# Kernel tuning notes

Measured on AMD Instinct MI355X. Metric: run time of the kernel, lower is better.

The kernel has to match this reference:

```python
import jax, jax.numpy as jnp
import numpy as np

CH = 512
NUM_GROUPS = 32
EPS = 1e-6

def _xavier(key, shape):
    fan_in, fan_out = shape[1], shape[0]
    limit = np.sqrt(6.0 / (fan_in + fan_out))
    return jax.random.uniform(key, shape, jnp.float32, -limit, limit)

def setup_inputs() -> dict:
    key = jax.random.key(0)
    ks = jax.random.split(key, 6)
    B, C, H, W = 32, CH, 32, 32
    x = jax.random.normal(ks[0], (B, C, H, W), jnp.float32)
    # 1x1 conv weights stored as [C_out, C_in]; biases zero (per initialize())
    wq = _xavier(ks[1], (C, C)); wk = _xavier(ks[2], (C, C))
    wv = _xavier(ks[3], (C, C)); wp = _xavier(ks[4], (C, C))
    bq = jnp.zeros((C,)); bk = jnp.zeros((C,)); bv = jnp.zeros((C,)); bp = jnp.zeros((C,))
    gn_w = jnp.ones((C,)); gn_b = jnp.zeros((C,))
    return {"x": x, "gn_w": gn_w, "gn_b": gn_b,
            "wq": wq, "bq": bq, "wk": wk, "bk": bk,
            "wv": wv, "bv": bv, "wp": wp, "bp": bp}

def _group_norm(x, w, b):
    B, C, H, W = x.shape
    g = NUM_GROUPS
    xg = x.reshape(B, g, C // g, H, W)
    mean = xg.mean(axis=(2, 3, 4), keepdims=True)
    var = xg.var(axis=(2, 3, 4), keepdims=True)
    xn = ((xg - mean) * jax.lax.rsqrt(var + EPS)).reshape(B, C, H, W)
    return xn * w[None, :, None, None] + b[None, :, None, None]

def reference(x, gn_w, gn_b, wq, bq, wk, bk, wv, bv, wp, bp):
    B, C, H, W = x.shape
    h = _group_norm(x, gn_w, gn_b)
    hf = h.reshape(B, C, H * W)  # [B, C, N]
    # 1x1 convs == per-pixel linear over channels
    q = jnp.einsum('oc,bcn->bno', wq, hf) + bq  # [B, N, C]
    k = jnp.einsum('oc,bcn->bon', wk, hf) + bk[None, :, None]  # [B, C, N]
    v = jnp.einsum('oc,bcn->bno', wv, hf) + bv  # [B, N, C]
    attn = jnp.einsum('bqc,bck->bqk', q, k) * (C ** -0.5)  # [B, N, N]
    attn = jax.nn.softmax(attn, axis=-1)
    out = jnp.einsum('bqk,bkc->bqc', attn, v)  # [B, N, C]
    out = jnp.einsum('oc,bnc->bon', wp, out) + bp[None, :, None]  # [B, C, N]
    return x + out.reshape(B, C, H, W)
```

## Files before the change

### kernel.cpp

```cpp
#include <hip/hip_runtime.h>


#define C_DIM 512
#define N_PIX 1024
#define BATCH 32
#define CPG 16
#define EPS 1e-6f
#define SCALE 0.044194173824159216f
#define ESTRIDE 66
#define ESTRU   72

typedef unsigned short u16;
typedef __attribute__((ext_vector_type(8))) short bf16x8;
typedef __attribute__((ext_vector_type(4))) float f32x4;
typedef __attribute__((ext_vector_type(2))) float f32x2;

static __device__ __forceinline__ float bf2f(u16 u) {
    union { unsigned int i; float f; } v; v.i = ((unsigned int)u) << 16; return v.f;
}
static __device__ __forceinline__ u16 f2bf(float f) {
    union { float f; unsigned int i; } v; v.f = f;
    unsigned int r = v.i + 0x7fffu + ((v.i >> 16) & 1u);
    return (u16)(r >> 16);
}

static __device__ __forceinline__ void gl_lds16(const u16* g, u16* l) {
    __builtin_amdgcn_global_load_lds(
        (const __attribute__((address_space(1))) unsigned int*)g,
        (__attribute__((address_space(3))) unsigned int*)l,
        16, 0, 0);
}

#define BAR()   __builtin_amdgcn_s_barrier()
#define SCHED() __builtin_amdgcn_sched_barrier(0x7)

__global__ __launch_bounds__(256) void prep_kernel(
        const float* __restrict__ wq, const float* __restrict__ wk,
        const float* __restrict__ wv, const float* __restrict__ wp,
        u16* __restrict__ out, const float* __restrict__ x,
        float* __restrict__ stats) {
    int blk = blockIdx.x;
    if (blk < 1024) {
        int i = blk * 256 + threadIdx.x;
        int mat = i >> 16;
        const float* src = (mat == 0) ? wq : (mat == 1) ? wk : (mat == 2) ? wv : wp;
        float4 v = ((const float4*)src)[i & 65535];
        ushort4 o;
        o.x = f2bf(v.x); o.y = f2bf(v.y); o.z = f2bf(v.z); o.w = f2bf(v.w);
        *(ushort4*)&out[(size_t)i * 4] = o;
        return;
    }
    blk -= 1024;
    int b = blk >> 5, g = blk & 31;
    const float4* xv = (const float4*)(x + ((size_t)(b * C_DIM + g * CPG)) * N_PIX);
    int tid = threadIdx.x;
    float s = 0.f, sq = 0.f;
#pragma unroll 4
    for (int i = tid; i < (CPG * N_PIX) / 4; i += 256) {
        float4 v = xv[i];
        s  += v.x + v.y + v.z + v.w;
        sq += v.x * v.x + v.y * v.y + v.z * v.z + v.w * v.w;
    }
#pragma unroll
    for (int m = 1; m < 64; m <<= 1) {
        s += __shfl_xor(s, m);
        sq += __shfl_xor(sq, m);
    }
    __shared__ float rs[4], rq[4];
    int wv_ = tid >> 6;
    if ((tid & 63) == 0) { rs[wv_] = s; rq[wv_] = sq; }
    __syncthreads();
    if (tid == 0) {
        float S = rs[0] + rs[1] + rs[2] + rs[3];
        float Q = rq[0] + rq[1] + rq[2] + rq[3];
        float mean = S * (1.0f / (CPG * N_PIX));
        float var  = Q * (1.0f / (CPG * N_PIX)) - mean * mean;
        stats[blk * 2] = mean;
        stats[blk * 2 + 1] = rsqrtf(var + EPS);
    }
}

__global__ __launch_bounds__(256) void gnt_kernel(
        const float* __restrict__ x, const float* __restrict__ gw,
        const float* __restrict__ gb, const float* __restrict__ stats,
        u16* __restrict__ h) {
    int blk = blockIdx.x;
    int b = blk >> 4, nc = blk & 15;
    int n0 = nc * 64;
    __shared__ u16 T[64 * 520];
    int tid = threadIdx.x;
    int cq = tid >> 4;
    int n4 = tid & 15;
    const float* xb = x + (size_t)b * C_DIM * N_PIX + n0;
#pragma unroll 4
    for (int pass = 0; pass < 32; ++pass) {
        int c = pass * 16 + cq;
        int g = c >> 4;
        float mean = stats[(b * 32 + g) * 2];
        float inv  = stats[(b * 32 + g) * 2 + 1];
        float sc = gw[c] * inv;
        float sh = gb[c] - mean * sc;
        float4 v = *(const float4*)(xb + (size_t)c * N_PIX + n4 * 4);
        int nn = n4 * 4;
        T[(nn + 0) * 520 + c] = f2bf(v.x * sc + sh);
        T[(nn + 1) * 520 + c] = f2bf(v.y * sc + sh);
        T[(nn + 2) * 520 + c] = f2bf(v.z * sc + sh);
        T[(nn + 3) * 520 + c] = f2bf(v.w * sc + sh);
    }
    __syncthreads();
    u16* hb = h + ((size_t)b * N_PIX + n0) * C_DIM;
    int rr = tid >> 5;
    int cc = (tid & 31) * 16;
#pragma unroll
    for (int p = 0; p < 8; ++p) {
        int n = p * 8 + rr;
        bf16x8 v0 = *(const bf16x8*)&T[n * 520 + cc];
        bf16x8 v1 = *(const bf16x8*)&T[n * 520 + cc + 8];
        *(bf16x8*)&hb[(size_t)n * C_DIM + cc] = v0;
        *(bf16x8*)&hb[(size_t)n * C_DIM + cc + 8] = v1;
    }
}


#define MM(mq, nq) do { \
    _Pragma("unroll") \
    for (int t_ = 0; t_ < 4; ++t_) { \
        _Pragma("unroll") \
        for (int n_ = 0; n_ < 2; ++n_) { \
            _Pragma("unroll") \
            for (int ks_ = 0; ks_ < 2; ++ks_) \
                acc[(mq)*4 + t_][(nq)*2 + n_] = \
                    __builtin_amdgcn_mfma_f32_16x16x32_bf16( \
                        af[t_][ks_], bf[(nq)*2 + n_][ks_], \
                        acc[(mq)*4 + t_][(nq)*2 + n_], 0, 0, 0); \
        } \
    } \
} while (0)

template <int MODE, int NT>
__global__ __launch_bounds__(512, 2) void gemm_kernel(
        const u16* __restrict__ A, const u16* __restrict__ A2,
        const u16* __restrict__ B, const u16* __restrict__ B2,
        void* __restrict__ Cv, void* __restrict__ Cv2,
        const float* __restrict__ bias, const float* __restrict__ bias2,
        const float* __restrict__ xres, int K,
        int rsA, int rsB, int rsC,
        long long bsA, long long bsB, long long bsC,
        int nx, int ny) {
    const int nwg = 256 * NT;

    const u16* tgA[2]; const u16* tgB[2];
    void* tout[2]; const float* tbi[2];
    int tcb[2], tcolb[2], trowb[2];
#pragma unroll
    for (int tt = 0; tt < NT; ++tt) {
        int flat = blockIdx.x + tt * 256;
        int t = (flat & 7) * (nwg >> 3) + (flat >> 3);
        int bx = t % nx, by = (t / nx) % ny, bz = t / (nx * ny);
        int b = bz;
        const u16 *gA, *gB;
        void* out = Cv;
        const float* bi = bias;
        if (MODE == 0) {
            int mat = bz & 1; b = bz >> 1;
            gA = A + (size_t)b * bsA + (size_t)by * 256 * rsA;
            gB = B + (size_t)mat * 262144 + (size_t)bx * 256 * rsB;
            out = mat ? Cv2 : Cv;
            bi = mat ? bias2 : bias;
        } else if (MODE == 2) {
            gA = A + (size_t)b * bsA + (size_t)by * 256 * rsA;
            gB = B + (size_t)b * bsB + (size_t)bx * 256 * rsB;
            out = (b >= 16) ? Cv2 : Cv;
        } else if (MODE == 3) {
            gA = ((b >= 16) ? A2 : A) + (size_t)(b & 15) * bsA + (size_t)by * 256 * rsA;
            gB = B + (size_t)b * bsB + (size_t)bx * 256 * rsB;
            out = (b >= 16) ? Cv2 : Cv;
        } else if (MODE == 4) {
            gA = A + (size_t)by * 256 * rsA;
            gB = ((b >= 16) ? B2 : B) + (size_t)(b & 15) * bsB + (size_t)bx * 256 * rsB;
        } else {
            gA = A + (size_t)by * 256 * rsA;
            gB = B + (size_t)b * bsB + (size_t)bx * 256 * rsB;
        }
        tgA[tt] = gA; tgB[tt] = gB; tout[tt] = out; tbi[tt] = bi;
        tcb[tt] = (MODE == 2 || MODE == 3) ? (b & 15) : b;
        tcolb[tt] = bx * 256; trowb[tt] = by * 256;
    }

    __shared__ __align__(16) u16 smem[65536];

    int tid = threadIdx.x;
    int lane = tid & 63, wave = tid >> 6;
    int wm = wave >> 2, wn = wave & 3;
    int quad = lane >> 4, l15 = lane & 15, l7 = lane & 7;
    int srow = tid >> 3;
    int lg = (tid & 7) ^ (srow & 7);

    const int nk = K >> 6;
    const int nit = nk >> 1;

    auto STG = [&](const u16* g, int rs, int buf, int isB, int hh, int kt) {
        const u16* src = g + (size_t)(hh * 128 + srow) * rs + (size_t)kt * 64 + lg * 8;
        u16* dst = &smem[buf * 32768 + isB * 16384 + (hh * 128 + srow) * 64 + (tid & 7) * 8];
        gl_lds16(src, dst);
        gl_lds16(src + (size_t)64 * rs, dst + 4096);
    };
    auto LDA = [&](int buf, int mq, int t_, int ks) -> bf16x8 {
        return *(const bf16x8*)&smem[buf * 32768 +
            (wm * 128 + mq * 64 + t_ * 16 + l15) * 64 + (((ks * 4 + quad) ^ l7) << 3)];
    };
    auto LDB = [&](int buf, int nt, int ks) -> bf16x8 {
        return *(const bf16x8*)&smem[buf * 32768 + 16384 +
            (wn * 64 + nt * 16 + l15) * 64 + (((ks * 4 + quad) ^ l7) << 3)];
    };

    f32x4 acc[8][4];
    bf16x8 af[4][2], bf[4][2];

#pragma unroll
    for (int tt = 0; tt < NT; ++tt) {
        const bool hn = (tt + 1 < NT);
        const u16* cA = tgA[tt];
        const u16* cB = tgB[tt];
        const u16* nA = tgA[hn ? tt + 1 : tt];
        const u16* nB = tgB[hn ? tt + 1 : tt];

        if (tt == 0) {
            STG(cB, rsB, 0, 1, 0, 0); STG(cB, rsB, 0, 1, 1, 0);
            STG(cA, rsA, 0, 0, 0, 0); STG(cA, rsA, 0, 0, 1, 0);
            STG(cB, rsB, 1, 1, 0, 1); STG(cB, rsB, 1, 1, 1, 1);
            asm volatile("s_waitcnt vmcnt(4)" ::: "memory");
            SCHED(); BAR(); SCHED();
        }

#pragma unroll
        for (int mt = 0; mt < 8; ++mt)
#pragma unroll
            for (int nt = 0; nt < 4; ++nt)
                acc[mt][nt] = (f32x4){0.f, 0.f, 0.f, 0.f};

        for (int it = 0; it < nit; ++it) {
            const bool s = (it + 1 < nit);
            const int k1 = 2 * it + 1, k2 = 2 * it + 2, k3 = 2 * it + 3;

#pragma unroll
            for (int t_ = 0; t_ < 4; ++t_)
#pragma unroll
                for (int ks = 0; ks < 2; ++ks) af[t_][ks] = LDA(0, 0, t_, ks);
#pragma unroll
            for (int n = 0; n < 2; ++n)
#pragma unroll
                for (int ks = 0; ks < 2; ++ks) bf[n][ks] = LDB(0, n, ks);
            STG(cA, rsA, 1, 0, 0, k1);
            SCHED(); BAR(); SCHED();
            __builtin_amdgcn_s_setprio(1); MM(0, 0); __builtin_amdgcn_s_setprio(0);
            SCHED(); BAR(); SCHED();

#pragma unroll
            for (int n = 2; n < 4; ++n)
#pragma unroll
                for (int ks = 0; ks < 2; ++ks) bf[n][ks] = LDB(0, n, ks);
            STG(cA, rsA, 1, 0, 1, k1);
            SCHED(); BAR(); SCHED();
            __builtin_amdgcn_s_setprio(1); MM(0, 1); __builtin_amdgcn_s_setprio(0);
            SCHED(); BAR(); SCHED();

#pragma unroll
            for (int t_ = 0; t_ < 4; ++t_)
#pragma unroll
                for (int ks = 0; ks < 2; ++ks) af[t_][ks] = LDA(0, 1, t_, ks);
            if (s) STG(cB, rsB, 0, 1, 0, k2);
            else if (hn) STG(nB, rsB, 0, 1, 0, 0);
            SCHED(); BAR(); SCHED();
            __builtin_amdgcn_s_setprio(1); MM(1, 1); __builtin_amdgcn_s_setprio(0);
            SCHED(); BAR(); SCHED();

            if (s) STG(cB, rsB, 0, 1, 1, k2);
            else if (hn) STG(nB, rsB, 0, 1, 1, 0);
            SCHED(); BAR(); SCHED();
            __builtin_amdgcn_s_setprio(1); MM(1, 0); __builtin_amdgcn_s_setprio(0);
            if (s || hn) asm volatile("s_waitcnt vmcnt(4)" ::: "memory");
            else         asm volatile("s_waitcnt vmcnt(0)" ::: "memory");
            SCHED(); BAR(); SCHED();

#pragma unroll
            for (int t_ = 0; t_ < 4; ++t_)
#pragma unroll
                for (int ks = 0; ks < 2; ++ks) af[t_][ks] = LDA(1, 0, t_, ks);
#pragma unroll
            for (int n = 0; n < 2; ++n)
#pragma unroll
                for (int ks = 0; ks < 2; ++ks) bf[n][ks] = LDB(1, n, ks);
            if (s) STG(cA, rsA, 0, 0, 0, k2);
            else if (hn) STG(nA, rsA, 0, 0, 0, 0);
            SCHED(); BAR(); SCHED();
            __builtin_amdgcn_s_setprio(1); MM(0, 0); __builtin_amdgcn_s_setprio(0);
            SCHED(); BAR(); SCHED();

#pragma unroll
            for (int n = 2; n < 4; ++n)
#pragma unroll
                for (int ks = 0; ks < 2; ++ks) bf[n][ks] = LDB(1, n, ks);
            if (s) STG(cA, rsA, 0, 0, 1, k2);
            else if (hn) STG(nA, rsA, 0, 0, 1, 0);
            SCHED(); BAR(); SCHED();
            __builtin_amdgcn_s_setprio(1); MM(0, 1); __builtin_amdgcn_s_setprio(0);
            SCHED(); BAR(); SCHED();

#pragma unroll
            for (int t_ = 0; t_ < 4; ++t_)
#pragma unroll
                for (int ks = 0; ks < 2; ++ks) af[t_][ks] = LDA(1, 1, t_, ks);
            if (s) STG(cB, rsB, 1, 1, 0, k3);
            else if (hn) STG(nB, rsB, 1, 1, 0, 1);
            SCHED(); BAR(); SCHED();
            __builtin_amdgcn_s_setprio(1); MM(1, 1); __builtin_amdgcn_s_setprio(0);
            SCHED(); BAR(); SCHED();

            if (s) STG(cB, rsB, 1, 1, 1, k3);
            else if (hn) STG(nB, rsB, 1, 1, 1, 1);
            SCHED(); BAR(); SCHED();
            __builtin_amdgcn_s_setprio(1); MM(1, 0); __builtin_amdgcn_s_setprio(0);
            if (s) asm volatile("s_waitcnt vmcnt(4)" ::: "memory");
            SCHED(); BAR(); SCHED();
        }

        int colb = tcolb[tt] + wn * 64;
        int rowb = trowb[tt] + wm * 128;
        void* out = tout[tt];
        const float* bi_p = tbi[tt];
        int cb = tcb[tt];

        if (MODE == 4) {
            float* ebw = (float*)(smem + 32768) + wave * (16 * ESTRIDE);
            int er = lane >> 4;
            int ec4 = (lane & 15) * 4;
#pragma unroll
            for (int mt = 0; mt < 8; ++mt) {
#pragma unroll
                for (int nt = 0; nt < 4; ++nt) {
                    f32x4 a = acc[mt][nt];
#pragma unroll
                    for (int reg = 0; reg < 4; ++reg)
                        ebw[(quad * 4 + reg) * ESTRIDE + nt * 16 + l15] = a[reg];
                }
#pragma unroll
                for (int j = 0; j < 4; ++j) {
                    int lr = er + 4 * j;
                    f32x2 v0 = *(f32x2*)&ebw[lr * ESTRIDE + ec4];
                    f32x2 v1 = *(f32x2*)&ebw[lr * ESTRIDE + ec4 + 2];
                    int gr = rowb + mt * 16 + lr;
                    int gc = colb + ec4;
                    size_t cidx = (size_t)cb * bsC + (size_t)gr * rsC + gc;
                    float bi = bi_p[gr];
                    float4 xr = *(const float4*)&xres[cidx];
                    float4 st = make_float4(v0.x + bi + xr.x, v0.y + bi + xr.y,
                                            v1.x + bi + xr.z, v1.y + bi + xr.w);
                    *(float4*)&((float*)out)[cidx] = st;
                }
            }
        } else {
            u16* ebw = (smem + 32768) + wave * (16 * ESTRU);
            int er = lane >> 3;
            int ec = (lane & 7) * 8;
            float bcol[4];
            if (MODE == 0) {
#pragma unroll
                for (int nt = 0; nt < 4; ++nt)
                    bcol[nt] = bi_p[colb + nt * 16 + l15];
            }
#pragma unroll
            for (int mt = 0; mt < 8; ++mt) {
                float4 brow;
                if (MODE == 1)
                    brow = *(const float4*)&bi_p[rowb + mt * 16 + quad * 4];
#pragma unroll
                for (int nt = 0; nt < 4; ++nt) {
                    f32x4 a = acc[mt][nt];
#pragma unroll
                    for (int reg = 0; reg < 4; ++reg) {
                        float fv = a[reg];
                        if (MODE == 0) fv += bcol[nt];
                        else if (MODE == 1) fv += ((const float*)&brow)[reg];
                        else if (MODE == 2) fv *= SCALE;
                        ebw[(quad * 4 + reg) * ESTRU + nt * 16 + l15] = f2bf(fv);
                    }
                }
#pragma unroll
                for (int j = 0; j < 2; ++j) {
                    int lr = er + 8 * j;
                    bf16x8 vv = *(const bf16x8*)&ebw[lr * ESTRU + ec];
                    int gr = rowb + mt * 16 + lr;
                    size_t cidx = (size_t)cb * bsC + (size_t)gr * rsC + colb + ec;
                    *(bf16x8*)&((u16*)out)[cidx] = vv;
                }
            }
        }

        if (hn) {
            SCHED();
            asm volatile("s_waitcnt vmcnt(20)" ::: "memory");
            BAR(); SCHED();
        }
    }
}

__global__ __launch_bounds__(256) void softmax_kernel(
        u16* __restrict__ S0, u16* __restrict__ S1) {
    int row = blockIdx.x * 4 + (threadIdx.x >> 6);
    int lane = threadIdx.x & 63;
    u16* p = ((row & 16384) ? S1 : S0) + (size_t)(row & 16383) * N_PIX + lane * 16;
    bf16x8 u0 = *(const bf16x8*)p;
    bf16x8 u1 = *(const bf16x8*)(p + 8);
    float f[16];
#pragma unroll
    for (int i = 0; i < 8; ++i) {
        f[i] = bf2f((u16)u0[i]);
        f[8 + i] = bf2f((u16)u1[i]);
    }
    float m = f[0];
#pragma unroll
    for (int i = 1; i < 16; ++i) m = fmaxf(m, f[i]);
#pragma unroll
    for (int off = 1; off < 64; off <<= 1) m = fmaxf(m, __shfl_xor(m, off));
    float s = 0.f;
#pragma unroll
    for (int i = 0; i < 16; ++i) { f[i] = __expf(f[i] - m); s += f[i]; }
#pragma unroll
    for (int off = 1; off < 64; off <<= 1) s += __shfl_xor(s, off);
    float inv = 1.0f / s;
    bf16x8 s0, s1;
#pragma unroll
    for (int i = 0; i < 8; ++i) {
        s0[i] = (short)f2bf(f[i] * inv);
        s1[i] = (short)f2bf(f[8 + i] * inv);
    }
    *(bf16x8*)p = s0;
    *(bf16x8*)(p + 8) = s1;
}

extern "C" void kernel_launch(void* const* d_in, const int* in_sizes, int n_in,
                              void* d_out, int out_size, void* d_ws, size_t ws_size,
                              hipStream_t stream) {
    const float* x    = (const float*)d_in[0];
    const float* gn_w = (const float*)d_in[1];
    const float* gn_b = (const float*)d_in[2];
    const float* wq   = (const float*)d_in[3];
    const float* bq   = (const float*)d_in[4];
    const float* wk   = (const float*)d_in[5];
    const float* bk   = (const float*)d_in[6];
    const float* wv   = (const float*)d_in[7];
    const float* bv   = (const float*)d_in[8];
    const float* wp   = (const float*)d_in[9];
    const float* bp   = (const float*)d_in[10];
    float* y = (float*)d_out;

    const size_t BCN = (size_t)BATCH * C_DIM * N_PIX;
    char* w = (char*)d_ws;
    u16* h  = (u16*)(w);
    u16* q  = (u16*)(w + 2 * BCN);
    u16* k  = (u16*)(w + 4 * BCN);
    u16* v  = (u16*)(w + 6 * BCN);
    u16* Or = (u16*)(w + 8 * BCN);
    u16* wb = (u16*)(w + 10 * BCN);
    u16* wvb = wb + 524288, *wpb = wb + 786432;
    float* stats = (float*)(w + 10 * BCN + 2 * 1024 * 1024);
    u16* S0 = h;
    u16* S1 = Or;
    u16* O0 = q;
    u16* O1 = k;

    const long long BS = 524288;
    const long long SB = 1048576;

    prep_kernel<<<2048, 256, 0, stream>>>(wq, wk, wv, wp, wb, x, stats);
    gnt_kernel<<<512, 256, 0, stream>>>(x, gn_w, gn_b, stats, h);

    gemm_kernel<0, 2><<<256, 512, 0, stream>>>(
        h, nullptr, wb, nullptr, q, k, bq, bk, nullptr,
        512, 512, 512, 512, BS, 0, BS, 2, 4);
    gemm_kernel<1, 1><<<256, 512, 0, stream>>>(
        wvb, nullptr, h, nullptr, v, nullptr, bv, nullptr, nullptr,
        512, 512, 512, 1024, 0, BS, BS, 4, 2);

    gemm_kernel<2, 2><<<256, 512, 0, stream>>>(
        q, nullptr, k, nullptr, S0, S1, nullptr, nullptr, nullptr,
        512, 512, 512, 1024, BS, BS, SB, 4, 4);
    softmax_kernel<<<8192, 256, 0, stream>>>(S0, S1);
    gemm_kernel<3, 1><<<256, 512, 0, stream>>>(
        S0, S1, v, nullptr, O0, O1, nullptr, nullptr, nullptr,
        1024, 1024, 1024, 512, SB, BS, BS, 2, 4);

    gemm_kernel<4, 1><<<256, 512, 0, stream>>>(
        wpb, nullptr, O0, O1, y, nullptr, bp, nullptr, x,
        512, 512, 512, 1024, 0, BS, BS, 4, 2);
}
```

Baseline: 341.1 us.

## Fuse softmax into QK^T epilogue and PV prologue via partial row stats

Removes the standalone softmax kernel, which read and rewrote the full bf16 score matrix. The QK^T GEMM epilogue now writes per-row partial max and sum-of-exp for each 64-column slice. A small combine kernel reduces these to a final max and inverse sum per row. The PV GEMM then loads raw scores through registers, applies exp and normalisation, and writes the result to LDS instead of using direct global-to-LDS loads. This saves one full read and write of S, but adds exp work and register pressure inside the GEMM's A-operand path and changes its load pipelining.

```diff
diff --git a/kernel.cpp b/kernel.cpp
--- a/kernel.cpp
+++ b/kernel.cpp
@@ -33,6 +33,7 @@
 
 #define BAR()   __builtin_amdgcn_s_barrier()
 #define SCHED() __builtin_amdgcn_sched_barrier(0x7)
+#define LGKM0() asm volatile("s_waitcnt lgkmcnt(0)" ::: "memory")
 
 __global__ __launch_bounds__(256) void prep_kernel(
         const float* __restrict__ wq, const float* __restrict__ wk,
@@ -121,6 +122,23 @@
     }
 }
 
+__global__ __launch_bounds__(256) void comb_kernel(
+        const float* __restrict__ pstat, float* __restrict__ sstat) {
+    int row = blockIdx.x * 16 + (threadIdx.x >> 4);
+    int p = threadIdx.x & 15;
+    f32x2 mp = *(const f32x2*)&pstat[((size_t)row * 16 + p) * 2];
+    float m = mp.x;
+#pragma unroll
+    for (int off = 1; off < 16; off <<= 1) m = fmaxf(m, __shfl_xor(m, off));
+    float s = mp.y * __expf(mp.x - m);
+#pragma unroll
+    for (int off = 1; off < 16; off <<= 1) s += __shfl_xor(s, off);
+    if (p == 0) {
+        f32x2 o; o.x = m; o.y = 1.0f / s;
+        *(f32x2*)&sstat[(size_t)row * 2] = o;
+    }
+}
+
 
 #define MM(mq, nq) do { \
     _Pragma("unroll") \
@@ -143,15 +161,17 @@
         const u16* __restrict__ B, const u16* __restrict__ B2,
         void* __restrict__ Cv, void* __restrict__ Cv2,
         const float* __restrict__ bias, const float* __restrict__ bias2,
-        const float* __restrict__ xres, int K,
+        const float* __restrict__ xres,
+        const float* __restrict__ sstat, float* __restrict__ pstat, int K,
         int rsA, int rsB, int rsC,
         long long bsA, long long bsB, long long bsC,
         int nx, int ny) {
     const int nwg = 256 * NT;
 
-    const u16* tgA[2]; const u16* tgB[2];
-    void* tout[2]; const float* tbi[2];
-    int tcb[2], tcolb[2], trowb[2];
+    const u16* tgA[NT]; const u16* tgB[NT];
+    void* tout[NT]; const float* tbi[NT];
+    const float* tst_[NT]; float* tps_[NT];
+    int tcb[NT], tcolb[NT], trowb[NT], tpart_[NT];
 #pragma unroll
     for (int tt = 0; tt < NT; ++tt) {
         int flat = blockIdx.x + tt * 256;
@@ -161,6 +181,7 @@
         const u16 *gA, *gB;
         void* out = Cv;
         const float* bi = bias;
+        tst_[tt] = nullptr; tps_[tt] = nullptr; tpart_[tt] = 0;
         if (MODE == 0) {
             int mat = bz & 1; b = bz >> 1;
             gA = A + (size_t)b * bsA + (size_t)by * 256 * rsA;
@@ -171,10 +192,13 @@
             gA = A + (size_t)b * bsA + (size_t)by * 256 * rsA;
             gB = B + (size_t)b * bsB + (size_t)bx * 256 * rsB;
             out = (b >= 16) ? Cv2 : Cv;
+            tps_[tt] = pstat + (size_t)b * 1024 * 32;
+            tpart_[tt] = bx * 4;
         } else if (MODE == 3) {
             gA = ((b >= 16) ? A2 : A) + (size_t)(b & 15) * bsA + (size_t)by * 256 * rsA;
             gB = B + (size_t)b * bsB + (size_t)bx * 256 * rsB;
             out = (b >= 16) ? Cv2 : Cv;
+            tst_[tt] = sstat + ((size_t)b * 1024 + (size_t)by * 256) * 2;
         } else if (MODE == 4) {
             gA = A + (size_t)by * 256 * rsA;
             gB = ((b >= 16) ? B2 : B) + (size_t)(b & 15) * bsB + (size_t)bx * 256 * rsB;
@@ -214,6 +238,35 @@
             (wn * 64 + nt * 16 + l15) * 64 + (((ks * 4 + quad) ^ l7) << 3)];
     };
 
+    uint4 ar0, ar1, ar2, ar3;
+    f32x2 sb0, sb1, sb2, sb3;
+    auto AISS = [&](const u16* cA, int kt, const float* stb) {
+        const u16* s0 = cA + (size_t)srow * rsA + (size_t)kt * 64 + lg * 8;
+        ar0 = *(const uint4*)s0;
+        ar1 = *(const uint4*)(s0 + (size_t)64 * rsA);
+        ar2 = *(const uint4*)(s0 + (size_t)128 * rsA);
+        ar3 = *(const uint4*)(s0 + (size_t)192 * rsA);
+        sb0 = *(const f32x2*)&stb[(size_t)srow * 2];
+        sb1 = *(const f32x2*)&stb[(size_t)(srow + 64) * 2];
+        sb2 = *(const f32x2*)&stb[(size_t)(srow + 128) * 2];
+        sb3 = *(const f32x2*)&stb[(size_t)(srow + 192) * 2];
+    };
+    auto XF = [&](uint4 r, f32x2 st) -> bf16x8 {
+        bf16x8 o;
+        const u16* e = (const u16*)&r;
+#pragma unroll
+        for (int i = 0; i < 8; ++i)
+            o[i] = (short)f2bf(__expf(bf2f(e[i]) - st.x) * st.y);
+        return o;
+    };
+    auto AWR = [&](int buf) {
+        u16* d = &smem[buf * 32768 + srow * 64 + (tid & 7) * 8];
+        *(bf16x8*)d = XF(ar0, sb0);
+        *(bf16x8*)(d + 4096) = XF(ar1, sb1);
+        *(bf16x8*)(d + 8192) = XF(ar2, sb2);
+        *(bf16x8*)(d + 12288) = XF(ar3, sb3);
+    };
+
     f32x4 acc[8][4];
     bf16x8 af[4][2], bf[4][2];
 
@@ -224,12 +277,21 @@
         const u16* cB = tgB[tt];
         const u16* nA = tgA[hn ? tt + 1 : tt];
         const u16* nB = tgB[hn ? tt + 1 : tt];
+        const float* stb = tst_[tt];
 
         if (tt == 0) {
-            STG(cB, rsB, 0, 1, 0, 0); STG(cB, rsB, 0, 1, 1, 0);
-            STG(cA, rsA, 0, 0, 0, 0); STG(cA, rsA, 0, 0, 1, 0);
-            STG(cB, rsB, 1, 1, 0, 1); STG(cB, rsB, 1, 1, 1, 1);
-            asm volatile("s_waitcnt vmcnt(4)" ::: "memory");
+            if (MODE == 3) {
+                STG(cB, rsB, 0, 1, 0, 0); STG(cB, rsB, 0, 1, 1, 0);
+                AISS(cA, 0, stb);
+                STG(cB, rsB, 1, 1, 0, 1); STG(cB, rsB, 1, 1, 1, 1);
+                AWR(0);
+                LGKM0();
+            } else {
+                STG(cB, rsB, 0, 1, 0, 0); STG(cB, rsB, 0, 1, 1, 0);
+                STG(cA, rsA, 0, 0, 0, 0); STG(cA, rsA, 0, 0, 1, 0);
+                STG(cB, rsB, 1, 1, 0, 1); STG(cB, rsB, 1, 1, 1, 1);
+                asm volatile("s_waitcnt vmcnt(4)" ::: "memory");
+            }
             SCHED(); BAR(); SCHED();
         }
 
@@ -251,7 +313,8 @@
             for (int n = 0; n < 2; ++n)
 #pragma unroll
                 for (int ks = 0; ks < 2; ++ks) bf[n][ks] = LDB(0, n, ks);
-            STG(cA, rsA, 1, 0, 0, k1);
+            if (MODE == 3) AISS(cA, k1, stb);
+            else STG(cA, rsA, 1, 0, 0, k1);
             SCHED(); BAR(); SCHED();
             __builtin_amdgcn_s_setprio(1); MM(0, 0); __builtin_amdgcn_s_setprio(0);
             SCHED(); BAR(); SCHED();
@@ -260,7 +323,8 @@
             for (int n = 2; n < 4; ++n)
 #pragma unroll
                 for (int ks = 0; ks < 2; ++ks) bf[n][ks] = LDB(0, n, ks);
-            STG(cA, rsA, 1, 0, 1, k1);
+            if (MODE == 3) AWR(1);
+            else STG(cA, rsA, 1, 0, 1, k1);
             SCHED(); BAR(); SCHED();
             __builtin_amdgcn_s_setprio(1); MM(0, 1); __builtin_amdgcn_s_setprio(0);
             SCHED(); BAR(); SCHED();
@@ -279,6 +343,7 @@
             else if (hn) STG(nB, rsB, 0, 1, 1, 0);
             SCHED(); BAR(); SCHED();
             __builtin_amdgcn_s_setprio(1); MM(1, 0); __builtin_amdgcn_s_setprio(0);
+            if (MODE == 3) LGKM0();
             if (s || hn) asm volatile("s_waitcnt vmcnt(4)" ::: "memory");
             else         asm volatile("s_waitcnt vmcnt(0)" ::: "memory");
             SCHED(); BAR(); SCHED();
@@ -291,7 +356,7 @@
             for (int n = 0; n < 2; ++n)
 #pragma unroll
                 for (int ks = 0; ks < 2; ++ks) bf[n][ks] = LDB(1, n, ks);
-            if (s) STG(cA, rsA, 0, 0, 0, k2);
+            if (s) { if (MODE == 3) AISS(cA, k2, stb); else STG(cA, rsA, 0, 0, 0, k2); }
             else if (hn) STG(nA, rsA, 0, 0, 0, 0);
             SCHED(); BAR(); SCHED();
             __builtin_amdgcn_s_setprio(1); MM(0, 0); __builtin_amdgcn_s_setprio(0);
@@ -301,7 +366,7 @@
             for (int n = 2; n < 4; ++n)
 #pragma unroll
                 for (int ks = 0; ks < 2; ++ks) bf[n][ks] = LDB(1, n, ks);
-            if (s) STG(cA, rsA, 0, 0, 1, k2);
+            if (s) { if (MODE == 3) AWR(0); else STG(cA, rsA, 0, 0, 1, k2); }
             else if (hn) STG(nA, rsA, 0, 0, 1, 0);
             SCHED(); BAR(); SCHED();
             __builtin_amdgcn_s_setprio(1); MM(0, 1); __builtin_amdgcn_s_setprio(0);
@@ -321,6 +386,7 @@
             else if (hn) STG(nB, rsB, 1, 1, 1, 1);
             SCHED(); BAR(); SCHED();
             __builtin_amdgcn_s_setprio(1); MM(1, 0); __builtin_amdgcn_s_setprio(0);
+            if (MODE == 3 && s) LGKM0();
             if (s) asm volatile("s_waitcnt vmcnt(4)" ::: "memory");
             SCHED(); BAR(); SCHED();
         }
@@ -395,48 +461,44 @@
                     *(bf16x8*)&((u16*)out)[cidx] = vv;
                 }
             }
+            if (MODE == 2) {
+                float* pb = tps_[tt];
+                int part = tpart_[tt] + wn;
+#pragma unroll
+                for (int mt = 0; mt < 8; ++mt) {
+#pragma unroll
+                    for (int reg = 0; reg < 4; ++reg) {
+                        float m = acc[mt][0][reg];
+#pragma unroll
+                        for (int nt = 1; nt < 4; ++nt) m = fmaxf(m, acc[mt][nt][reg]);
+                        m *= SCALE;
+#pragma unroll
+                        for (int off = 1; off < 16; off <<= 1)
+                            m = fmaxf(m, __shfl_xor(m, off));
+                        float sm = 0.f;
+#pragma unroll
+                        for (int nt = 0; nt < 4; ++nt)
+                            sm += __expf(acc[mt][nt][reg] * SCALE - m);
+#pragma unroll
+                        for (int off = 1; off < 16; off <<= 1)
+                            sm += __shfl_xor(sm, off);
+                        if (l15 == 0) {
+                            int gr = rowb + mt * 16 + quad * 4 + reg;
+                            f32x2 o; o.x = m; o.y = sm;
+                            *(f32x2*)&pb[((size_t)gr * 16 + part) * 2] = o;
+                        }
+                    }
+                }
+            }
         }
 
         if (hn) {
             SCHED();
-            asm volatile("s_waitcnt vmcnt(20)" ::: "memory");
+            if (MODE == 2) asm volatile("s_waitcnt vmcnt(4)" ::: "memory");
+            else           asm volatile("s_waitcnt vmcnt(20)" ::: "memory");
             BAR(); SCHED();
         }
     }
-}
-
-__global__ __launch_bounds__(256) void softmax_kernel(
-        u16* __restrict__ S0, u16* __restrict__ S1) {
-    int row = blockIdx.x * 4 + (threadIdx.x >> 6);
-    int lane = threadIdx.x & 63;
-    u16* p = ((row & 16384) ? S1 : S0) + (size_t)(row & 16383) * N_PIX + lane * 16;
-    bf16x8 u0 = *(const bf16x8*)p;
-    bf16x8 u1 = *(const bf16x8*)(p + 8);
-    float f[16];
-#pragma unroll
-    for (int i = 0; i < 8; ++i) {
-        f[i] = bf2f((u16)u0[i]);
-        f[8 + i] = bf2f((u16)u1[i]);
-    }
-    float m = f[0];
-#pragma unroll
-    for (int i = 1; i < 16; ++i) m = fmaxf(m, f[i]);
-#pragma unroll
-    for (int off = 1; off < 64; off <<= 1) m = fmaxf(m, __shfl_xor(m, off));
-    float s = 0.f;
-#pragma unroll
-    for (int i = 0; i < 16; ++i) { f[i] = __expf(f[i] - m); s += f[i]; }
-#pragma unroll
-    for (int off = 1; off < 64; off <<= 1) s += __shfl_xor(s, off);
-    float inv = 1.0f / s;
-    bf16x8 s0, s1;
-#pragma unroll
-    for (int i = 0; i < 8; ++i) {
-        s0[i] = (short)f2bf(f[i] * inv);
-        s1[i] = (short)f2bf(f[8 + i] * inv);
-    }
-    *(bf16x8*)p = s0;
-    *(bf16x8*)(p + 8) = s1;
 }
 
 extern "C" void kernel_launch(void* const* d_in, const int* in_sizes, int n_in,
@@ -465,6 +527,8 @@
     u16* wb = (u16*)(w + 10 * BCN);
     u16* wvb = wb + 524288, *wpb = wb + 786432;
     float* stats = (float*)(w + 10 * BCN + 2 * 1024 * 1024);
+    float* pst   = (float*)(w + 10 * BCN + 2 * 1024 * 1024 + 65536);
+    float* sst   = pst + (size_t)32 * 1024 * 16 * 2;
     u16* S0 = h;
     u16* S1 = Or;
     u16* O0 = q;
@@ -477,21 +541,21 @@
     gnt_kernel<<<512, 256, 0, stream>>>(x, gn_w, gn_b, stats, h);
 
     gemm_kernel<0, 2><<<256, 512, 0, stream>>>(
-        h, nullptr, wb, nullptr, q, k, bq, bk, nullptr,
+        h, nullptr, wb, nullptr, q, k, bq, bk, nullptr, nullptr, nullptr,
         512, 512, 512, 512, BS, 0, BS, 2, 4);
     gemm_kernel<1, 1><<<256, 512, 0, stream>>>(
-        wvb, nullptr, h, nullptr, v, nullptr, bv, nullptr, nullptr,
+        wvb, nullptr, h, nullptr, v, nullptr, bv, nullptr, nullptr, nullptr, nullptr,
         512, 512, 512, 1024, 0, BS, BS, 4, 2);
 
     gemm_kernel<2, 2><<<256, 512, 0, stream>>>(
-        q, nullptr, k, nullptr, S0, S1, nullptr, nullptr, nullptr,
+        q, nullptr, k, nullptr, S0, S1, nullptr, nullptr, nullptr, nullptr, pst,
         512, 512, 512, 1024, BS, BS, SB, 4, 4);
-    softmax_kernel<<<8192, 256, 0, stream>>>(S0, S1);
+    comb_kernel<<<2048, 256, 0, stream>>>(pst, sst);
     gemm_kernel<3, 1><<<256, 512, 0, stream>>>(
-        S0, S1, v, nullptr, O0, O1, nullptr, nullptr, nullptr,
+        S0, S1, v, nullptr, O0, O1, nullptr, nullptr, nullptr, sst, nullptr,
         1024, 1024, 1024, 512, SB, BS, BS, 2, 4);
 
     gemm_kernel<4, 1><<<256, 512, 0, stream>>>(
-        wpb, nullptr, O0, O1, y, nullptr, bp, nullptr, x,
+        wpb, nullptr, O0, O1, y, nullptr, bp, nullptr, x, nullptr, nullptr,
         512, 512, 512, 1024, 0, BS, BS, 4, 2);
 }
```

Measured after the change: 431.3 us. +26.5%, slower.

## Add smaller-tile GEMM kernel for QK projection and score GEMMs

Applied to the files above, without the earlier changes.

Adds a gemm32_kernel that uses 256x128 output tiles with a K-step of 32, a smaller LDS footprint and launch bounds allowing 4 blocks per CU. It launches 1024 blocks instead of 256 persistent blocks that each processed two tiles. It is used for the Q/K projection and the QK^T score GEMM. The original kernel loses its multi-tile (NT) persistence path, so cross-tile prefetch goes away. The aim is higher occupancy and more workgroups for better latency hiding and load balance, at the cost of less data reuse per tile and more LDS synchronisation per unit of work.

```diff
diff --git a/kernel.cpp b/kernel.cpp
--- a/kernel.cpp
+++ b/kernel.cpp
@@ -9,6 +9,7 @@
 #define SCALE 0.044194173824159216f
 #define ESTRIDE 66
 #define ESTRU   72
+#define ES2     40
 
 typedef unsigned short u16;
 typedef __attribute__((ext_vector_type(8))) short bf16x8;
@@ -122,6 +123,165 @@
 }
 
 
+#define MM32(mq) do { \
+    _Pragma("unroll") \
+    for (int t_ = 0; t_ < 4; ++t_) { \
+        _Pragma("unroll") \
+        for (int n_ = 0; n_ < 2; ++n_) \
+            acc[(mq)*4 + t_][n_] = \
+                __builtin_amdgcn_mfma_f32_16x16x32_bf16( \
+                    af[t_], bf[n_], acc[(mq)*4 + t_][n_], 0, 0, 0); \
+    } \
+} while (0)
+
+template <int MODE>
+__global__ __launch_bounds__(512, 4) void gemm32_kernel(
+        const u16* __restrict__ A, const u16* __restrict__ B,
+        void* __restrict__ Cv, void* __restrict__ Cv2,
+        const float* __restrict__ bias, const float* __restrict__ bias2,
+        int K, int rsA, int rsB, int rsC,
+        long long bsA, long long bsB, long long bsC) {
+    int flat = blockIdx.x;
+    int t = (flat & 7) * 128 + (flat >> 3);
+
+    const u16 *gA, *gB;
+    void* out;
+    const float* bi_p;
+    int cb, colb, rowb;
+    if (MODE == 0) {
+        int bx = t & 3, by = (t >> 2) & 3, z = t >> 4;
+        int mat = z & 1, b = z >> 1;
+        gA = A + (size_t)b * bsA + (size_t)by * 256 * rsA;
+        gB = B + (size_t)mat * 262144 + (size_t)bx * 128 * rsB;
+        out = mat ? Cv2 : Cv;
+        bi_p = mat ? bias2 : bias;
+        cb = b; colb = bx * 128; rowb = by * 256;
+    } else {
+        int bx = t & 7, by = (t >> 3) & 3, b = t >> 5;
+        gA = A + (size_t)b * bsA + (size_t)by * 256 * rsA;
+        gB = B + (size_t)b * bsB + (size_t)bx * 128 * rsB;
+        out = (b >= 16) ? Cv2 : Cv;
+        bi_p = nullptr;
+        cb = b & 15; colb = bx * 128; rowb = by * 256;
+    }
+
+    __shared__ __align__(16) u16 smem[24576];
+
+    int tid = threadIdx.x;
+    int lane = tid & 63, wave = tid >> 6;
+    int wm = wave >> 2, wn = wave & 3;
+    int quad = lane >> 4, l15 = lane & 15;
+    int srow = tid >> 2;
+    int lg = (tid & 3) ^ ((srow >> 1) & 3);
+
+    const int nk = K >> 5;
+    const int nit = nk >> 1;
+
+    auto STGA = [&](int buf, int hh, int kt) {
+        const u16* src = gA + (size_t)(hh * 128 + srow) * rsA + (size_t)kt * 32 + lg * 8;
+        u16* dst = &smem[buf * 12288 + (hh * 128 + srow) * 32 + (tid & 3) * 8];
+        gl_lds16(src, dst);
+    };
+    auto STGB = [&](int buf, int kt) {
+        const u16* src = gB + (size_t)srow * rsB + (size_t)kt * 32 + lg * 8;
+        u16* dst = &smem[buf * 12288 + 8192 + srow * 32 + (tid & 3) * 8];
+        gl_lds16(src, dst);
+    };
+    auto LDA32 = [&](int buf, int mq, int t_) -> bf16x8 {
+        int r = wm * 128 + mq * 64 + t_ * 16 + l15;
+        return *(const bf16x8*)&smem[buf * 12288 + r * 32 +
+                                     ((quad ^ ((r >> 1) & 3)) << 3)];
+    };
+    auto LDB32 = [&](int buf, int nt) -> bf16x8 {
+        int r = wn * 32 + nt * 16 + l15;
+        return *(const bf16x8*)&smem[buf * 12288 + 8192 + r * 32 +
+                                     ((quad ^ ((r >> 1) & 3)) << 3)];
+    };
+
+    f32x4 acc[8][2];
+#pragma unroll
+    for (int mt = 0; mt < 8; ++mt)
+#pragma unroll
+        for (int nt = 0; nt < 2; ++nt)
+            acc[mt][nt] = (f32x4){0.f, 0.f, 0.f, 0.f};
+    bf16x8 af[4], bf[2];
+
+    STGA(0, 0, 0); STGA(0, 1, 0); STGB(0, 0); STGB(1, 1);
+    asm volatile("s_waitcnt vmcnt(1)" ::: "memory");
+    SCHED(); BAR(); SCHED();
+
+    for (int it = 0; it < nit; ++it) {
+        const bool s = (it + 1 < nit);
+        const int k1 = 2 * it + 1, k2 = 2 * it + 2, k3 = 2 * it + 3;
+
+#pragma unroll
+        for (int t_ = 0; t_ < 4; ++t_) af[t_] = LDA32(0, 0, t_);
+#pragma unroll
+        for (int n = 0; n < 2; ++n) bf[n] = LDB32(0, n);
+        STGA(1, 0, k1); STGA(1, 1, k1);
+        SCHED(); BAR(); SCHED();
+        __builtin_amdgcn_s_setprio(1); MM32(0); __builtin_amdgcn_s_setprio(0);
+        SCHED(); BAR(); SCHED();
+
+#pragma unroll
+        for (int t_ = 0; t_ < 4; ++t_) af[t_] = LDA32(0, 1, t_);
+        if (s) STGB(0, k2);
+        SCHED(); BAR(); SCHED();
+        __builtin_amdgcn_s_setprio(1); MM32(1); __builtin_amdgcn_s_setprio(0);
+        if (s) asm volatile("s_waitcnt vmcnt(1)" ::: "memory");
+        else   asm volatile("s_waitcnt vmcnt(0)" ::: "memory");
+        SCHED(); BAR(); SCHED();
+
+#pragma unroll
+        for (int t_ = 0; t_ < 4; ++t_) af[t_] = LDA32(1, 0, t_);
+#pragma unroll
+        for (int n = 0; n < 2; ++n) bf[n] = LDB32(1, n);
+        if (s) { STGA(0, 0, k2); STGA(0, 1, k2); }
+        SCHED(); BAR(); SCHED();
+        __builtin_amdgcn_s_setprio(1); MM32(0); __builtin_amdgcn_s_setprio(0);
+        SCHED(); BAR(); SCHED();
+
+#pragma unroll
+        for (int t_ = 0; t_ < 4; ++t_) af[t_] = LDA32(1, 1, t_);
+        if (s) STGB(1, k3);
+        SCHED(); BAR(); SCHED();
+        __builtin_amdgcn_s_setprio(1); MM32(1); __builtin_amdgcn_s_setprio(0);
+        if (s) asm volatile("s_waitcnt vmcnt(1)" ::: "memory");
+        SCHED(); BAR(); SCHED();
+    }
+
+    int colb_w = colb + wn * 32;
+    int rowb_w = rowb + wm * 128;
+    u16* ebw = smem + wave * (16 * ES2);
+    int lr = lane >> 2;
+    int ec = (lane & 3) * 8;
+    float bcol[2];
+    if (MODE == 0) {
+#pragma unroll
+        for (int nt = 0; nt < 2; ++nt)
+            bcol[nt] = bi_p[colb_w + nt * 16 + l15];
+    }
+#pragma unroll
+    for (int mt = 0; mt < 8; ++mt) {
+#pragma unroll
+        for (int nt = 0; nt < 2; ++nt) {
+            f32x4 a = acc[mt][nt];
+#pragma unroll
+            for (int reg = 0; reg < 4; ++reg) {
+                float fv = a[reg];
+                if (MODE == 0) fv += bcol[nt];
+                else fv *= SCALE;
+                ebw[(quad * 4 + reg) * ES2 + nt * 16 + l15] = f2bf(fv);
+            }
+        }
+        bf16x8 vv = *(const bf16x8*)&ebw[lr * ES2 + ec];
+        size_t cidx = (size_t)cb * bsC + (size_t)(rowb_w + mt * 16 + lr) * rsC
+                      + colb_w + ec;
+        *(bf16x8*)&((u16*)out)[cidx] = vv;
+    }
+}
+
+
 #define MM(mq, nq) do { \
     _Pragma("unroll") \
     for (int t_ = 0; t_ < 4; ++t_) { \
@@ -137,55 +297,33 @@
     } \
 } while (0)
 
-template <int MODE, int NT>
+template <int MODE>
 __global__ __launch_bounds__(512, 2) void gemm_kernel(
         const u16* __restrict__ A, const u16* __restrict__ A2,
         const u16* __restrict__ B, const u16* __restrict__ B2,
         void* __restrict__ Cv, void* __restrict__ Cv2,
-        const float* __restrict__ bias, const float* __restrict__ bias2,
-        const float* __restrict__ xres, int K,
-        int rsA, int rsB, int rsC,
+        const float* __restrict__ bias, const float* __restrict__ xres,
+        int K, int rsA, int rsB, int rsC,
         long long bsA, long long bsB, long long bsC,
         int nx, int ny) {
-    const int nwg = 256 * NT;
-
-    const u16* tgA[2]; const u16* tgB[2];
-    void* tout[2]; const float* tbi[2];
-    int tcb[2], tcolb[2], trowb[2];
-#pragma unroll
-    for (int tt = 0; tt < NT; ++tt) {
-        int flat = blockIdx.x + tt * 256;
-        int t = (flat & 7) * (nwg >> 3) + (flat >> 3);
-        int bx = t % nx, by = (t / nx) % ny, bz = t / (nx * ny);
-        int b = bz;
-        const u16 *gA, *gB;
-        void* out = Cv;
-        const float* bi = bias;
-        if (MODE == 0) {
-            int mat = bz & 1; b = bz >> 1;
-            gA = A + (size_t)b * bsA + (size_t)by * 256 * rsA;
-            gB = B + (size_t)mat * 262144 + (size_t)bx * 256 * rsB;
-            out = mat ? Cv2 : Cv;
-            bi = mat ? bias2 : bias;
-        } else if (MODE == 2) {
-            gA = A + (size_t)b * bsA + (size_t)by * 256 * rsA;
-            gB = B + (size_t)b * bsB + (size_t)bx * 256 * rsB;
-            out = (b >= 16) ? Cv2 : Cv;
-        } else if (MODE == 3) {
-            gA = ((b >= 16) ? A2 : A) + (size_t)(b & 15) * bsA + (size_t)by * 256 * rsA;
-            gB = B + (size_t)b * bsB + (size_t)bx * 256 * rsB;
-            out = (b >= 16) ? Cv2 : Cv;
-        } else if (MODE == 4) {
-            gA = A + (size_t)by * 256 * rsA;
-            gB = ((b >= 16) ? B2 : B) + (size_t)(b & 15) * bsB + (size_t)bx * 256 * rsB;
-        } else {
-            gA = A + (size_t)by * 256 * rsA;
-            gB = B + (size_t)b * bsB + (size_t)bx * 256 * rsB;
-        }
-        tgA[tt] = gA; tgB[tt] = gB; tout[tt] = out; tbi[tt] = bi;
-        tcb[tt] = (MODE == 2 || MODE == 3) ? (b & 15) : b;
-        tcolb[tt] = bx * 256; trowb[tt] = by * 256;
-    }
+    int flat = blockIdx.x;
+    int t = (flat & 7) * 32 + (flat >> 3);
+    int bx = t % nx, by = (t / nx) % ny, bz = t / (nx * ny);
+    int b = bz;
+    const u16 *gA, *gB;
+    void* out = Cv;
+    if (MODE == 3) {
+        gA = ((b >= 16) ? A2 : A) + (size_t)(b & 15) * bsA + (size_t)by * 256 * rsA;
+        gB = B + (size_t)b * bsB + (size_t)bx * 256 * rsB;
+        out = (b >= 16) ? Cv2 : Cv;
+    } else if (MODE == 4) {
+        gA = A + (size_t)by * 256 * rsA;
+        gB = ((b >= 16) ? B2 : B) + (size_t)(b & 15) * bsB + (size_t)bx * 256 * rsB;
+    } else {
+        gA = A + (size_t)by * 256 * rsA;
+        gB = B + (size_t)b * bsB + (size_t)bx * 256 * rsB;
+    }
+    int cb = (MODE == 3) ? (b & 15) : b;
 
     __shared__ __align__(16) u16 smem[65536];
 
@@ -215,192 +353,157 @@
     };
 
     f32x4 acc[8][4];
+#pragma unroll
+    for (int mt = 0; mt < 8; ++mt)
+#pragma unroll
+        for (int nt = 0; nt < 4; ++nt)
+            acc[mt][nt] = (f32x4){0.f, 0.f, 0.f, 0.f};
     bf16x8 af[4][2], bf[4][2];
 
-#pragma unroll
-    for (int tt = 0; tt < NT; ++tt) {
-        const bool hn = (tt + 1 < NT);
-        const u16* cA = tgA[tt];
-        const u16* cB = tgB[tt];
-        const u16* nA = tgA[hn ? tt + 1 : tt];
-        const u16* nB = tgB[hn ? tt + 1 : tt];
-
-        if (tt == 0) {
-            STG(cB, rsB, 0, 1, 0, 0); STG(cB, rsB, 0, 1, 1, 0);
-            STG(cA, rsA, 0, 0, 0, 0); STG(cA, rsA, 0, 0, 1, 0);
-            STG(cB, rsB, 1, 1, 0, 1); STG(cB, rsB, 1, 1, 1, 1);
-            asm volatile("s_waitcnt vmcnt(4)" ::: "memory");
-            SCHED(); BAR(); SCHED();
+    STG(gB, rsB, 0, 1, 0, 0); STG(gB, rsB, 0, 1, 1, 0);
+    STG(gA, rsA, 0, 0, 0, 0); STG(gA, rsA, 0, 0, 1, 0);
+    STG(gB, rsB, 1, 1, 0, 1); STG(gB, rsB, 1, 1, 1, 1);
+    asm volatile("s_waitcnt vmcnt(4)" ::: "memory");
+    SCHED(); BAR(); SCHED();
+
+    for (int it = 0; it < nit; ++it) {
+        const bool s = (it + 1 < nit);
+        const int k1 = 2 * it + 1, k2 = 2 * it + 2, k3 = 2 * it + 3;
+
+#pragma unroll
+        for (int t_ = 0; t_ < 4; ++t_)
+#pragma unroll
+            for (int ks = 0; ks < 2; ++ks) af[t_][ks] = LDA(0, 0, t_, ks);
+#pragma unroll
+        for (int n = 0; n < 2; ++n)
+#pragma unroll
+            for (int ks = 0; ks < 2; ++ks) bf[n][ks] = LDB(0, n, ks);
+        STG(gA, rsA, 1, 0, 0, k1);
+        SCHED(); BAR(); SCHED();
+        __builtin_amdgcn_s_setprio(1); MM(0, 0); __builtin_amdgcn_s_setprio(0);
+        SCHED(); BAR(); SCHED();
+
+#pragma unroll
+        for (int n = 2; n < 4; ++n)
+#pragma unroll
+            for (int ks = 0; ks < 2; ++ks) bf[n][ks] = LDB(0, n, ks);
+        STG(gA, rsA, 1, 0, 1, k1);
+        SCHED(); BAR(); SCHED();
+        __builtin_amdgcn_s_setprio(1); MM(0, 1); __builtin_amdgcn_s_setprio(0);
+        SCHED(); BAR(); SCHED();
+
+#pragma unroll
+        for (int t_ = 0; t_ < 4; ++t_)
+#pragma unroll
+            for (int ks = 0; ks < 2; ++ks) af[t_][ks] = LDA(0, 1, t_, ks);
+        if (s) STG(gB, rsB, 0, 1, 0, k2);
+        SCHED(); BAR(); SCHED();
+        __builtin_amdgcn_s_setprio(1); MM(1, 1); __builtin_amdgcn_s_setprio(0);
+        SCHED(); BAR(); SCHED();
+
+        if (s) STG(gB, rsB, 0, 1, 1, k2);
+        SCHED(); BAR(); SCHED();
+        __builtin_amdgcn_s_setprio(1); MM(1, 0); __builtin_amdgcn_s_setprio(0);
+        if (s) asm volatile("s_waitcnt vmcnt(4)" ::: "memory");
+        else   asm volatile("s_waitcnt vmcnt(0)" ::: "memory");
+        SCHED(); BAR(); SCHED();
+
+#pragma unroll
+        for (int t_ = 0; t_ < 4; ++t_)
+#pragma unroll
+            for (int ks = 0; ks < 2; ++ks) af[t_][ks] = LDA(1, 0, t_, ks);
+#pragma unroll
+        for (int n = 0; n < 2; ++n)
+#pragma unroll
+            for (int ks = 0; ks < 2; ++ks) bf[n][ks] = LDB(1, n, ks);
+        if (s) STG(gA, rsA, 0, 0, 0, k2);
+        SCHED(); BAR(); SCHED();
+        __builtin_amdgcn_s_setprio(1); MM(0, 0); __builtin_amdgcn_s_setprio(0);
+        SCHED(); BAR(); SCHED();
+
+#pragma unroll
+        for (int n = 2; n < 4; ++n)
+#pragma unroll
+            for (int ks = 0; ks < 2; ++ks) bf[n][ks] = LDB(1, n, ks);
+        if (s) STG(gA, rsA, 0, 0, 1, k2);
+        SCHED(); BAR(); SCHED();
+        __builtin_amdgcn_s_setprio(1); MM(0, 1); __builtin_amdgcn_s_setprio(0);
+        SCHED(); BAR(); SCHED();
+
+#pragma unroll
+        for (int t_ = 0; t_ < 4; ++t_)
+#pragma unroll
+            for (int ks = 0; ks < 2; ++ks) af[t_][ks] = LDA(1, 1, t_, ks);
+        if (s) STG(gB, rsB, 1, 1, 0, k3);
+        SCHED(); BAR(); SCHED();
+        __builtin_amdgcn_s_setprio(1); MM(1, 1); __builtin_amdgcn_s_setprio(0);
+        SCHED(); BAR(); SCHED();
+
+        if (s) STG(gB, rsB, 1, 1, 1, k3);
+        SCHED(); BAR(); SCHED();
+        __builtin_amdgcn_s_setprio(1); MM(1, 0); __builtin_amdgcn_s_setprio(0);
+        if (s) asm volatile("s_waitcnt vmcnt(4)" ::: "memory");
+        SCHED(); BAR(); SCHED();
+    }
+
+    int colb = bx * 256 + wn * 64;
+    int rowb = by * 256 + wm * 128;
+
+    if (MODE == 4) {
+        float* ebw = (float*)(smem + 32768) + wave * (16 * ESTRIDE);
+        int er = lane >> 4;
+        int ec4 = (lane & 15) * 4;
+#pragma unroll
+        for (int mt = 0; mt < 8; ++mt) {
+#pragma unroll
+            for (int nt = 0; nt < 4; ++nt) {
+                f32x4 a = acc[mt][nt];
+#pragma unroll
+                for (int reg = 0; reg < 4; ++reg)
+                    ebw[(quad * 4 + reg) * ESTRIDE + nt * 16 + l15] = a[reg];
+            }
+#pragma unroll
+            for (int j = 0; j < 4; ++j) {
+                int lr = er + 4 * j;
+                f32x2 v0 = *(f32x2*)&ebw[lr * ESTRIDE + ec4];
+                f32x2 v1 = *(f32x2*)&ebw[lr * ESTRIDE + ec4 + 2];
+                int gr = rowb + mt * 16 + lr;
+                int gc = colb + ec4;
+                size_t cidx = (size_t)cb * bsC + (size_t)gr * rsC + gc;
+                float bi = bias[gr];
+                float4 xr = *(const float4*)&xres[cidx];
+                float4 st = make_float4(v0.x + bi + xr.x, v0.y + bi + xr.y,
+                                        v1.x + bi + xr.z, v1.y + bi + xr.w);
+                *(float4*)&((float*)out)[cidx] = st;
+            }
         }
-
-#pragma unroll
-        for (int mt = 0; mt < 8; ++mt)
-#pragma unroll
-            for (int nt = 0; nt < 4; ++nt)
-                acc[mt][nt] = (f32x4){0.f, 0.f, 0.f, 0.f};
-
-        for (int it = 0; it < nit; ++it) {
-            const bool s = (it + 1 < nit);
-            const int k1 = 2 * it + 1, k2 = 2 * it + 2, k3 = 2 * it + 3;
-
-#pragma unroll
-            for (int t_ = 0; t_ < 4; ++t_)
-#pragma unroll
-                for (int ks = 0; ks < 2; ++ks) af[t_][ks] = LDA(0, 0, t_, ks);
-#pragma unroll
-            for (int n = 0; n < 2; ++n)
-#pragma unroll
-                for (int ks = 0; ks < 2; ++ks) bf[n][ks] = LDB(0, n, ks);
-            STG(cA, rsA, 1, 0, 0, k1);
-            SCHED(); BAR(); SCHED();
-            __builtin_amdgcn_s_setprio(1); MM(0, 0); __builtin_amdgcn_s_setprio(0);
-            SCHED(); BAR(); SCHED();
-
-#pragma unroll
-            for (int n = 2; n < 4; ++n)
-#pragma unroll
-                for (int ks = 0; ks < 2; ++ks) bf[n][ks] = LDB(0, n, ks);
-            STG(cA, rsA, 1, 0, 1, k1);
-            SCHED(); BAR(); SCHED();
-            __builtin_amdgcn_s_setprio(1); MM(0, 1); __builtin_amdgcn_s_setprio(0);
-            SCHED(); BAR(); SCHED();
-
-#pragma unroll
-            for (int t_ = 0; t_ < 4; ++t_)
-#pragma unroll
-                for (int ks = 0; ks < 2; ++ks) af[t_][ks] = LDA(0, 1, t_, ks);
-            if (s) STG(cB, rsB, 0, 1, 0, k2);
-            else if (hn) STG(nB, rsB, 0, 1, 0, 0);
-            SCHED(); BAR(); SCHED();
-            __builtin_amdgcn_s_setprio(1); MM(1, 1); __builtin_amdgcn_s_setprio(0);
-            SCHED(); BAR(); SCHED();
-
-            if (s) STG(cB, rsB, 0, 1, 1, k2);
-            else if (hn) STG(nB, rsB, 0, 1, 1, 0);
-            SCHED(); BAR(); SCHED();
-            __builtin_amdgcn_s_setprio(1); MM(1, 0); __builtin_amdgcn_s_setprio(0);
-            if (s || hn) asm volatile("s_waitcnt vmcnt(4)" ::: "memory");
-            else         asm volatile("s_waitcnt vmcnt(0)" ::: "memory");
-            SCHED(); BAR(); SCHED();
-
-#pragma unroll
-            for (int t_ = 0; t_ < 4; ++t_)
-#pragma unroll
-                for (int ks = 0; ks < 2; ++ks) af[t_][ks] = LDA(1, 0, t_, ks);
-#pragma unroll
-            for (int n = 0; n < 2; ++n)
-#pragma unroll
-                for (int ks = 0; ks < 2; ++ks) bf[n][ks] = LDB(1, n, ks);
-            if (s) STG(cA, rsA, 0, 0, 0, k2);
-            else if (hn) STG(nA, rsA, 0, 0, 0, 0);
-            SCHED(); BAR(); SCHED();
-            __builtin_amdgcn_s_setprio(1); MM(0, 0); __builtin_amdgcn_s_setprio(0);
-            SCHED(); BAR(); SCHED();
-
-#pragma unroll
-            for (int n = 2; n < 4; ++n)
-#pragma unroll
-                for (int ks = 0; ks < 2; ++ks) bf[n][ks] = LDB(1, n, ks);
-            if (s) STG(cA, rsA, 0, 0, 1, k2);
-            else if (hn) STG(nA, rsA, 0, 0, 1, 0);
-            SCHED(); BAR(); SCHED();
-            __builtin_amdgcn_s_setprio(1); MM(0, 1); __builtin_amdgcn_s_setprio(0);
-            SCHED(); BAR(); SCHED();
-
-#pragma unroll
-            for (int t_ = 0; t_ < 4; ++t_)
-#pragma unroll
-                for (int ks = 0; ks < 2; ++ks) af[t_][ks] = LDA(1, 1, t_, ks);
-            if (s) STG(cB, rsB, 1, 1, 0, k3);
-            else if (hn) STG(nB, rsB, 1, 1, 0, 1);
-            SCHED(); BAR(); SCHED();
-            __builtin_amdgcn_s_setprio(1); MM(1, 1); __builtin_amdgcn_s_setprio(0);
-            SCHED(); BAR(); SCHED();
-
-            if (s) STG(cB, rsB, 1, 1, 1, k3);
-            else if (hn) STG(nB, rsB, 1, 1, 1, 1);
-            SCHED(); BAR(); SCHED();
-            __builtin_amdgcn_s_setprio(1); MM(1, 0); __builtin_amdgcn_s_setprio(0);
-            if (s) asm volatile("s_waitcnt vmcnt(4)" ::: "memory");
-            SCHED(); BAR(); SCHED();
-        }
-
-        int colb = tcolb[tt] + wn * 64;
-        int rowb = trowb[tt] + wm * 128;
-        void* out = tout[tt];
-        const float* bi_p = tbi[tt];
-        int cb = tcb[tt];
-
-        if (MODE == 4) {
-            float* ebw = (float*)(smem + 32768) + wave * (16 * ESTRIDE);
-            int er = lane >> 4;
-            int ec4 = (lane & 15) * 4;
-#pragma unroll
-            for (int mt = 0; mt < 8; ++mt) {
-#pragma unroll
-                for (int nt = 0; nt < 4; ++nt) {
-                    f32x4 a = acc[mt][nt];
-#pragma unroll
-                    for (int reg = 0; reg < 4; ++reg)
-                        ebw[(quad * 4 + reg) * ESTRIDE + nt * 16 + l15] = a[reg];
-                }
-#pragma unroll
-                for (int j = 0; j < 4; ++j) {
-                    int lr = er + 4 * j;
-                    f32x2 v0 = *(f32x2*)&ebw[lr * ESTRIDE + ec4];
-                    f32x2 v1 = *(f32x2*)&ebw[lr * ESTRIDE + ec4 + 2];
-                    int gr = rowb + mt * 16 + lr;
-                    int gc = colb + ec4;
-                    size_t cidx = (size_t)cb * bsC + (size_t)gr * rsC + gc;
-                    float bi = bi_p[gr];
-                    float4 xr = *(const float4*)&xres[cidx];
-                    float4 st = make_float4(v0.x + bi + xr.x, v0.y + bi + xr.y,
-                                            v1.x + bi + xr.z, v1.y + bi + xr.w);
-                    *(float4*)&((float*)out)[cidx] = st;
+    } else {
+        u16* ebw = (smem + 32768) + wave * (16 * ESTRU);
+        int er = lane >> 3;
+        int ec = (lane & 7) * 8;
+#pragma unroll
+        for (int mt = 0; mt < 8; ++mt) {
+            float4 brow = make_float4(0.f, 0.f, 0.f, 0.f);
+            if (MODE == 1)
+                brow = *(const float4*)&bias[rowb + mt * 16 + quad * 4];
+#pragma unroll
+            for (int nt = 0; nt < 4; ++nt) {
+                f32x4 a = acc[mt][nt];
+#pragma unroll
+                for (int reg = 0; reg < 4; ++reg) {
+                    float fv = a[reg];
+                    if (MODE == 1) fv += ((const float*)&brow)[reg];
+                    ebw[(quad * 4 + reg) * ESTRU + nt * 16 + l15] = f2bf(fv);
                 }
             }
-        } else {
-            u16* ebw = (smem + 32768) + wave * (16 * ESTRU);
-            int er = lane >> 3;
-            int ec = (lane & 7) * 8;
-            float bcol[4];
-            if (MODE == 0) {
-#pragma unroll
-                for (int nt = 0; nt < 4; ++nt)
-                    bcol[nt] = bi_p[colb + nt * 16 + l15];
+#pragma unroll
+            for (int j = 0; j < 2; ++j) {
+                int lr = er + 8 * j;
+                bf16x8 vv = *(const bf16x8*)&ebw[lr * ESTRU + ec];
+                int gr = rowb + mt * 16 + lr;
+                size_t cidx = (size_t)cb * bsC + (size_t)gr * rsC + colb + ec;
+                *(bf16x8*)&((u16*)out)[cidx] = vv;
             }
-#pragma unroll
-            for (int mt = 0; mt < 8; ++mt) {
-                float4 brow;
-                if (MODE == 1)
-                    brow = *(const float4*)&bi_p[rowb + mt * 16 + quad * 4];
-#pragma unroll
-                for (int nt = 0; nt < 4; ++nt) {
-                    f32x4 a = acc[mt][nt];
-#pragma unroll
-                    for (int reg = 0; reg < 4; ++reg) {
-                        float fv = a[reg];
-                        if (MODE == 0) fv += bcol[nt];
-                        else if (MODE == 1) fv += ((const float*)&brow)[reg];
-                        else if (MODE == 2) fv *= SCALE;
-                        ebw[(quad * 4 + reg) * ESTRU + nt * 16 + l15] = f2bf(fv);
-                    }
-                }
-#pragma unroll
-                for (int j = 0; j < 2; ++j) {
-                    int lr = er + 8 * j;
-                    bf16x8 vv = *(const bf16x8*)&ebw[lr * ESTRU + ec];
-                    int gr = rowb + mt * 16 + lr;
-                    size_t cidx = (size_t)cb * bsC + (size_t)gr * rsC + colb + ec;
-                    *(bf16x8*)&((u16*)out)[cidx] = vv;
-                }
-            }
-        }
-
-        if (hn) {
-            SCHED();
-            asm volatile("s_waitcnt vmcnt(20)" ::: "memory");
-            BAR(); SCHED();
         }
     }
 }
@@ -476,22 +579,20 @@
     prep_kernel<<<2048, 256, 0, stream>>>(wq, wk, wv, wp, wb, x, stats);
     gnt_kernel<<<512, 256, 0, stream>>>(x, gn_w, gn_b, stats, h);
 
-    gemm_kernel<0, 2><<<256, 512, 0, stream>>>(
-        h, nullptr, wb, nullptr, q, k, bq, bk, nullptr,
-        512, 512, 512, 512, BS, 0, BS, 2, 4);
-    gemm_kernel<1, 1><<<256, 512, 0, stream>>>(
-        wvb, nullptr, h, nullptr, v, nullptr, bv, nullptr, nullptr,
+    gemm32_kernel<0><<<1024, 512, 0, stream>>>(
+        h, wb, q, k, bq, bk, 512, 512, 512, 512, BS, 0, BS);
+    gemm_kernel<1><<<256, 512, 0, stream>>>(
+        wvb, nullptr, h, nullptr, v, nullptr, bv, nullptr,
         512, 512, 512, 1024, 0, BS, BS, 4, 2);
 
-    gemm_kernel<2, 2><<<256, 512, 0, stream>>>(
-        q, nullptr, k, nullptr, S0, S1, nullptr, nullptr, nullptr,
-        512, 512, 512, 1024, BS, BS, SB, 4, 4);
+    gemm32_kernel<2><<<1024, 512, 0, stream>>>(
+        q, k, S0, S1, nullptr, nullptr, 512, 512, 512, 1024, BS, BS, SB);
     softmax_kernel<<<8192, 256, 0, stream>>>(S0, S1);
-    gemm_kernel<3, 1><<<256, 512, 0, stream>>>(
-        S0, S1, v, nullptr, O0, O1, nullptr, nullptr, nullptr,
+    gemm_kernel<3><<<256, 512, 0, stream>>>(
+        S0, S1, v, nullptr, O0, O1, nullptr, nullptr,
         1024, 1024, 1024, 512, SB, BS, BS, 2, 4);
 
-    gemm_kernel<4, 1><<<256, 512, 0, stream>>>(
-        wpb, nullptr, O0, O1, y, nullptr, bp, nullptr, x,
+    gemm_kernel<4><<<256, 512, 0, stream>>>(
+        wpb, nullptr, O0, O1, y, nullptr, bp, x,
         512, 512, 512, 1024, 0, BS, BS, 4, 2);
 }
```

Measured after the change: 337.6 us. About the same (-1.0%).
